# Kernel optimization log

Hardware: AMD Instinct MI355X
Metric: run time of the kernel (lower is better)

The kernel has to match this reference:

```python
import jax, jax.numpy as jnp
import numpy as np

RANK = 16
SHAPE = (512, 512, 512)


def setup_inputs() -> dict:
    key = jax.random.key(0)
    k0, k1, k2 = jax.random.split(key, 3)
    # factors initialized like torch.randn(rank, n_dim) / 100.0
    f0 = jax.random.normal(k0, (RANK, SHAPE[0]), dtype=jnp.float32) / 100.0
    f1 = jax.random.normal(k1, (RANK, SHAPE[1]), dtype=jnp.float32) / 100.0
    f2 = jax.random.normal(k2, (RANK, SHAPE[2]), dtype=jnp.float32) / 100.0
    return {"f0": f0, "f1": f1, "f2": f2}


def reference(f0, f1, f2):
    # CP/PARAFAC reconstruction: sum over rank of outer products.
    # Equivalent to torch.einsum('ka,kb,kc->abc', f0, f1, f2).
    # Expressed so XLA contracts (ka,kb->abk) via GEMM then (abk,kc->abc):
    return jnp.einsum('ka,kb,kc->abc', f0, f1, f2)
```

## Files before the change

### kernel.cpp

```cpp
#include <hip/hip_runtime.h>

#define RANK 16
#define N 512
#define ROWS 256

typedef float vfloat4 __attribute__((ext_vector_type(4)));

__global__ __launch_bounds__(256) void parafac_kernel(
    const float* __restrict__ f0,
    const float* __restrict__ f1,
    const float* __restrict__ f2,
    float* __restrict__ out)
{
    __shared__ float pt[ROWS][RANK];

    const int t    = threadIdx.x;
    const int wave = t >> 6;
    const int lane = t & 63;
    const int blk  = blockIdx.x;
    const int a    = blk >> 1;
    const int bb0  = (blk & 1) * ROWS;

    {
        const int b = bb0 + t;
#pragma unroll
        for (int k = 0; k < RANK; ++k)
            pt[t][k] = f0[k * N + a] * f1[k * N + b];
    }

    const int c4 = (wave & 1) * 256 + lane * 4;
    vfloat4 v[RANK];
#pragma unroll
    for (int k = 0; k < RANK; ++k)
        v[k] = *reinterpret_cast<const vfloat4*>(&f2[k * N + c4]);

    __syncthreads();

    const int rofs = wave >> 1;
    float* outb = out + ((size_t)a * N + bb0) * N + c4;

#pragma unroll 2
    for (int it = 0; it < ROWS / 2; ++it) {
        const int r = it * 2 + rofs;
        vfloat4 p0 = *reinterpret_cast<const vfloat4*>(&pt[r][0]);
        vfloat4 p1 = *reinterpret_cast<const vfloat4*>(&pt[r][4]);
        vfloat4 p2 = *reinterpret_cast<const vfloat4*>(&pt[r][8]);
        vfloat4 p3 = *reinterpret_cast<const vfloat4*>(&pt[r][12]);

        vfloat4 acc = (vfloat4)(0.f);
#pragma unroll
        for (int j = 0; j < 4; ++j) {
            acc += p0[j] * v[j];
            acc += p1[j] * v[4 + j];
            acc += p2[j] * v[8 + j];
            acc += p3[j] * v[12 + j];
        }
        *reinterpret_cast<vfloat4*>(outb + (size_t)r * N) = acc;
    }
}

extern "C" void kernel_launch(void* const* d_in, const int* in_sizes, int n_in,
                              void* d_out, int out_size, void* d_ws, size_t ws_size,
                              hipStream_t stream) {
    const float* f0 = (const float*)d_in[0];
    const float* f1 = (const float*)d_in[1];
    const float* f2 = (const float*)d_in[2];
    float* out = (float*)d_out;

    dim3 grid(N * 2);
    dim3 block(256);
    parafac_kernel<<<grid, block, 0, stream>>>(f0, f1, f2, out);
}
```

Baseline: 106.9 us.

## Drop shared-memory product table; compute f0*f1 per wave with strided row assignment

Removes the shared-memory table of f0*f1 products and the block barrier. Each wave-pair now keeps one b row of f1 in registers and loops over a with a stride of four, recomputing f0[k,a]*f1[k,b] on the fly from cached global loads. Output rows are spread across the whole tensor with a large stride, and launch bounds now request 4 blocks per CU. The kernel is bound by output stores, so moving the writes to non-contiguous rows and adding scalar loads plus extra multiplies inside the loop may hurt store locality.

```diff
diff --git a/kernel.cpp b/kernel.cpp
--- a/kernel.cpp
+++ b/kernel.cpp
@@ -2,60 +2,46 @@
 
 #define RANK 16
 #define N 512
-#define ROWS 256
 
 typedef float vfloat4 __attribute__((ext_vector_type(4)));
 
-__global__ __launch_bounds__(256) void parafac_kernel(
+__global__ __launch_bounds__(256, 4) void parafac_kernel(
     const float* __restrict__ f0,
     const float* __restrict__ f1,
     const float* __restrict__ f2,
     float* __restrict__ out)
 {
-    __shared__ float pt[ROWS][RANK];
-
     const int t    = threadIdx.x;
     const int wave = t >> 6;
     const int lane = t & 63;
-    const int blk  = blockIdx.x;
-    const int a    = blk >> 1;
-    const int bb0  = (blk & 1) * ROWS;
+    const int wp   = blockIdx.x * 2 + (wave >> 1);
+    const int b    = wp & (N - 1);
+    const int a0   = wp >> 9;
+    const int c4   = (wave & 1) * 256 + lane * 4;
 
-    {
-        const int b = bb0 + t;
+    float f1b[RANK];
 #pragma unroll
-        for (int k = 0; k < RANK; ++k)
-            pt[t][k] = f0[k * N + a] * f1[k * N + b];
-    }
+    for (int k = 0; k < RANK; ++k) f1b[k] = f1[k * N + b];
 
-    const int c4 = (wave & 1) * 256 + lane * 4;
     vfloat4 v[RANK];
 #pragma unroll
     for (int k = 0; k < RANK; ++k)
         v[k] = *reinterpret_cast<const vfloat4*>(&f2[k * N + c4]);
 
-    __syncthreads();
+    float* o = out + (size_t)wp * N + c4;
 
-    const int rofs = wave >> 1;
-    float* outb = out + ((size_t)a * N + bb0) * N + c4;
-
+    int a = a0;
 #pragma unroll 2
-    for (int it = 0; it < ROWS / 2; ++it) {
-        const int r = it * 2 + rofs;
-        vfloat4 p0 = *reinterpret_cast<const vfloat4*>(&pt[r][0]);
-        vfloat4 p1 = *reinterpret_cast<const vfloat4*>(&pt[r][4]);
-        vfloat4 p2 = *reinterpret_cast<const vfloat4*>(&pt[r][8]);
-        vfloat4 p3 = *reinterpret_cast<const vfloat4*>(&pt[r][12]);
-
+    for (int j = 0; j < 128; ++j) {
         vfloat4 acc = (vfloat4)(0.f);
 #pragma unroll
-        for (int j = 0; j < 4; ++j) {
-            acc += p0[j] * v[j];
-            acc += p1[j] * v[4 + j];
-            acc += p2[j] * v[8 + j];
-            acc += p3[j] * v[12 + j];
+        for (int k = 0; k < RANK; ++k) {
+            const float pk = f0[k * N + a] * f1b[k];
+            acc += pk * v[k];
         }
-        *reinterpret_cast<vfloat4*>(outb + (size_t)r * N) = acc;
+        *reinterpret_cast<vfloat4*>(o) = acc;
+        o += (size_t)2048 * N;
+        a += 4;
     }
 }
 
@@ -67,7 +53,7 @@
     const float* f2 = (const float*)d_in[2];
     float* out = (float*)d_out;
 
-    dim3 grid(N * 2);
+    dim3 grid(1024);
     dim3 block(256);
     parafac_kernel<<<grid, block, 0, stream>>>(f0, f1, f2, out);
 }
```

Measured after the change: 128.0 us. +19.7%, slower.
